# Optimization experiments

Hardware: AMD Instinct MI355X
Metric: run time of the kernel (lower is better)

## Reference

```python
import jax, jax.numpy as jnp
import numpy as np

D_MODEL = 1024
D_HIDDEN = 4096
N_EXPERTS = 8
N_TOKENS = 4096


def setup_inputs() -> dict:
    key = jax.random.key(0)
    ks = jax.random.split(key, 7)
    s = 0.02
    return {
        "x": jax.random.normal(ks[0], (N_TOKENS, D_MODEL), dtype=jnp.float32),
        "gate_w": jax.random.normal(ks[1], (N_EXPERTS, D_MODEL), dtype=jnp.float32) * s,
        "gate_b": jnp.zeros((N_EXPERTS,), dtype=jnp.float32),
        "w1": jax.random.normal(ks[2], (N_EXPERTS, D_MODEL, D_HIDDEN), dtype=jnp.float32) * s,
        "b1": jnp.zeros((N_EXPERTS, D_HIDDEN), dtype=jnp.float32),
        "w2": jax.random.normal(ks[3], (N_EXPERTS, D_HIDDEN, D_MODEL), dtype=jnp.float32) * s,
        "b2": jnp.zeros((N_EXPERTS, D_MODEL), dtype=jnp.float32),
    }


def reference(x, gate_w, gate_b, w1, b1, w2, b2):
    # gate: softmax over expert logits, hard top-1 routing (no prob weighting,
    # matching the torch module which writes the raw expert output back)
    gate_logits = x @ gate_w.T + gate_b                      # [N, E]
    gate_probs = jax.nn.softmax(gate_logits, axis=-1)
    top_expert = jnp.argmax(gate_probs, axis=-1)             # [N] int

    # dense all-expert MLP, then one-hot select (vectorized top-1 MoE)
    h = jax.nn.relu(jnp.einsum('nd,edh->neh', x, w1) + b1[None])  # [N, E, Dh]
    y = jnp.einsum('neh,ehd->ned', h, w2) + b2[None]              # [N, E, D]
    onehot = jax.nn.one_hot(top_expert, N_EXPERTS, dtype=x.dtype)  # [N, E]
    out = jnp.einsum('ned,ne->nd', y, onehot)                      # [N, D]
    return out
```

## Files before the change

kernel.cpp:

```cpp
#include <hip/hip_runtime.h>
#include <hip/hip_bf16.h>

#define NT 4096
#define DM 1024
#define DH 4096
#define NE 8

#define BM 128
#define BN 128
#define BK 32
#define MAXT 40
#define MAXROWS 5120
#define KSPL2 2
#define BKP 40
#define G1B (8 * 4 * MAXT)

typedef short bf16x8 __attribute__((ext_vector_type(8)));
typedef float f32x4 __attribute__((ext_vector_type(4)));
typedef float f4 __attribute__((ext_vector_type(4)));
typedef unsigned short u16x8 __attribute__((ext_vector_type(8)));

#define MI_COUNTS 0
#define MI_POFF   16
#define MI_NTILES 32
#define MI_TILEE  48
#define MI_TILER  112
#define MI_TILES0 176

#define O_BUCKET 1024ull
#define O_XB  (O_BUCKET + (size_t)NE * NT * 4)
#define O_H   (O_XB + (size_t)NT * DM * 2)
#define O_W1T (O_H + (size_t)MAXROWS * DH * 2)
#define O_W2T (O_W1T + (size_t)NE * DM * DH * 2)
#define WS_NEED (O_W2T + (size_t)NE * DH * DM * 2)
#define O_P   O_W1T

static __device__ __forceinline__ unsigned short f2bf(float f) {
  union { __hip_bfloat16 h; unsigned short u; } cv;
  cv.h = __float2bfloat16(f);
  return cv.u;
}

static __device__ __forceinline__ void gload16(const void* g, void* l) {
  __builtin_amdgcn_global_load_lds(
      (const __attribute__((address_space(1))) void*)g,
      (__attribute__((address_space(3))) void*)l, 16, 0, 0);
}

static __device__ __forceinline__ void convert_tile(
    const float* __restrict__ S, __hip_bfloat16* __restrict__ D, int K, int N,
    int k0, int n0, char* smem) {
  auto Ls = reinterpret_cast<__hip_bfloat16(*)[136]>(smem);
  const int tid = threadIdx.x;
  const int c = tid & 15, kq = tid >> 4;
  const float* src = S + (size_t)(k0 + kq * 8) * N + n0 + c * 4;
  f4 v[8];
#pragma unroll
  for (int j = 0; j < 8; ++j) v[j] = *(const f4*)(src + (size_t)j * N);
#pragma unroll
  for (int i = 0; i < 4; ++i) {
    u16x8 w;
#pragma unroll
    for (int j = 0; j < 8; ++j) w[j] = f2bf(v[j][i]);
    *(u16x8*)&Ls[c * 4 + i][kq * 8] = w;
  }
  __syncthreads();
  const int r = tid >> 2, q = tid & 3;
  __hip_bfloat16* drow = D + (size_t)(n0 + r) * K + k0 + q * 32;
#pragma unroll
  for (int u = 0; u < 4; ++u) {
    uint4 w = *(const uint4*)&Ls[r][q * 32 + u * 8];
    *(uint4*)(drow + u * 8) = w;
  }
}

static __device__ __forceinline__ void gate_body(
    const float* __restrict__ x, const float* __restrict__ gw,
    const float* __restrict__ gb, int* __restrict__ counts,
    int* __restrict__ bucket, __hip_bfloat16* __restrict__ xb, int bid) {
  const int tid = threadIdx.x;
  const int wid = tid >> 6;
  const int lane = tid & 63;
  const int t = bid * 4 + wid;

  const f4* xrow = (const f4*)(x + (size_t)t * DM);
  ushort4* xbrow = (ushort4*)(xb + (size_t)t * DM);

  double part[NE];
#pragma unroll
  for (int e = 0; e < NE; ++e) part[e] = 0.0;

#pragma unroll
  for (int q = 0; q < 4; ++q) {
    f4 v = xrow[q * 64 + lane];
    ushort4 s;
    s.x = f2bf(v[0]); s.y = f2bf(v[1]); s.z = f2bf(v[2]); s.w = f2bf(v[3]);
    xbrow[q * 64 + lane] = s;
#pragma unroll
    for (int e = 0; e < NE; ++e) {
      f4 w = ((const f4*)(gw + (size_t)e * DM))[q * 64 + lane];
      part[e] += (double)v[0] * w[0] + (double)v[1] * w[1] +
                 (double)v[2] * w[2] + (double)v[3] * w[3];
    }
  }
#pragma unroll
  for (int off = 32; off; off >>= 1) {
#pragma unroll
    for (int e = 0; e < NE; ++e) part[e] += __shfl_down(part[e], off);
  }
  if (lane == 0) {
    double best = part[0] + (double)gb[0];
    int bi = 0;
#pragma unroll
    for (int e = 1; e < NE; ++e) {
      double le = part[e] + (double)gb[e];
      if (le > best) { best = le; bi = e; }
    }
    int pos = atomicAdd(&counts[bi], 1);
    bucket[bi * NT + pos] = t;
  }
}

__global__ __launch_bounds__(256) void gate_cw1_kernel(
    const float* __restrict__ x, const float* __restrict__ gw,
    const float* __restrict__ gb, int* __restrict__ counts,
    int* __restrict__ bucket, __hip_bfloat16* __restrict__ xb,
    const float* __restrict__ w1, __hip_bfloat16* __restrict__ w1t) {
  __shared__ __align__(16) char smem[17408];
  const int bid = blockIdx.x;
  if (bid < NT / 4) {
    gate_body(x, gw, gb, counts, bucket, xb, bid);
    return;
  }
  const int id = bid - NT / 4;
  const int e = id >> 9, rem = id & 511;
  convert_tile(w1 + (size_t)e * DM * DH, w1t + (size_t)e * DM * DH, DM, DH,
               (rem >> 6) * 128, (rem & 63) * 64, smem);
}

__global__ void prefix_kernel(int* __restrict__ meta, int* __restrict__ bucket) {
  if (threadIdx.x == 0) {
    int r = 0, nt = 0;
    for (int e = 0; e < NE; ++e) {
      meta[MI_POFF + e] = r;
      const int cnt = meta[MI_COUNTS + e];
      const int T = (cnt + BM - 1) / BM;
      for (int j = 0; j < T; ++j) {
        meta[MI_TILEE + nt] = e;
        meta[MI_TILER + nt] = r + j * BM;
        meta[MI_TILES0 + nt] = j * BM;
        ++nt;
      }
      r += T * BM;
    }
    meta[MI_POFF + NE] = r;
    meta[MI_NTILES] = nt;
  }
  __syncthreads();
  for (int e = 0; e < NE; ++e) {
    const int cnt = meta[MI_COUNTS + e];
    if (cnt == 0) continue;
    const int padTo = ((cnt + BM - 1) / BM) * BM;
    const int last = bucket[e * NT + cnt - 1];
    for (int i = cnt + threadIdx.x; i < padTo; i += blockDim.x)
      bucket[e * NT + i] = last;
  }
}

template <int MODE>
static __device__ __forceinline__ void gemm_body(
    char* smem, int b, const __hip_bfloat16* __restrict__ A,
    const __hip_bfloat16* __restrict__ B, const float* __restrict__ biasAll,
    const int* __restrict__ meta, const int* __restrict__ bucket,
    void* __restrict__ Out) {
  auto As = reinterpret_cast<__hip_bfloat16(*)[BM][BK]>(smem);
  auto Bs = reinterpret_cast<__hip_bfloat16(*)[BN][BK]>(smem + 16384);

  const int xcd = b & 7;
  const int idx = b >> 3;
  int tile, ntile, kq;
  if (MODE == 0) {
    const int grp = idx / MAXT;
    tile = idx - grp * MAXT;
    ntile = xcd * 4 + grp;
    kq = 0;
  } else {
    const int grp = idx / MAXT;
    tile = idx - grp * MAXT;
    const int np = xcd * 2 + grp;
    ntile = np >> 1;
    kq = np & 1;
  }
  if (tile >= meta[MI_NTILES]) return;

  const int e = meta[MI_TILEE + tile];
  const int row0 = meta[MI_TILER + tile];
  const int s0 = meta[MI_TILES0 + tile];
  const int n0 = ntile * BN;
  const int Ktot = (MODE == 0) ? DM : DH;
  const int N = (MODE == 0) ? DH : DM;
  const int KTM = (MODE == 0) ? 32 : 64;
  const int kbase = (MODE == 0) ? 0 : kq * (DH / KSPL2);

  const int tid = threadIdx.x;
  const int lane = tid & 63;
  const int wid = tid >> 6;
  const int lr = lane >> 2, lc = lane & 3;

  const __hip_bfloat16 *aP0, *aP1;
  if (MODE == 0) {
    aP0 = A + (size_t)bucket[e * NT + s0 + 32 * wid + lr] * DM + lc * 8;
    aP1 = A + (size_t)bucket[e * NT + s0 + 32 * wid + 16 + lr] * DM + lc * 8;
  } else {
    aP0 = A + (size_t)(row0 + 32 * wid + lr) * DH + kbase + lc * 8;
    aP1 = A + (size_t)(row0 + 32 * wid + 16 + lr) * DH + kbase + lc * 8;
  }
  const __hip_bfloat16* bP0 =
      B + ((size_t)e * N + n0 + 32 * wid + lr) * Ktot + kbase + lc * 8;
  const __hip_bfloat16* bP1 = bP0 + (size_t)16 * Ktot;

  const int wm = (wid >> 1) * 64, wn = (wid & 1) * 64;
  const int fr = lane & 15, ks = lane >> 4;

  f32x4 acc[4][4];
#pragma unroll
  for (int m = 0; m < 4; ++m)
#pragma unroll
    for (int n = 0; n < 4; ++n) acc[m][n] = (f32x4){0.f, 0.f, 0.f, 0.f};

#define STAGE(bf, kt)                                  \
  do {                                                 \
    const size_t ko_ = (size_t)(kt) * BK;              \
    gload16(aP0 + ko_, &As[bf][32 * wid][0]);          \
    gload16(aP1 + ko_, &As[bf][32 * wid + 16][0]);     \
    gload16(bP0 + ko_, &Bs[bf][32 * wid][0]);          \
    gload16(bP1 + ko_, &Bs[bf][32 * wid + 16][0]);     \
  } while (0)

  STAGE(0, 0);
  __syncthreads();

  for (int kt = 0; kt < KTM; ++kt) {
    const int buf = kt & 1;
    if (kt + 1 < KTM) STAGE(buf ^ 1, kt + 1);
    bf16x8 afr[4], bfr[4];
#pragma unroll
    for (int m = 0; m < 4; ++m)
      afr[m] = *(const bf16x8*)&As[buf][wm + m * 16 + fr][ks * 8];
#pragma unroll
    for (int n = 0; n < 4; ++n)
      bfr[n] = *(const bf16x8*)&Bs[buf][wn + n * 16 + fr][ks * 8];
#pragma unroll
    for (int m = 0; m < 4; ++m)
#pragma unroll
      for (int n = 0; n < 4; ++n)
        acc[m][n] = __builtin_amdgcn_mfma_f32_16x16x32_bf16(afr[m], bfr[n],
                                                            acc[m][n], 0, 0, 0);
    __syncthreads();
  }
#undef STAGE

  if (MODE == 0) {
    const float* bias = biasAll + (size_t)e * DH;
    __hip_bfloat16* Hout = (__hip_bfloat16*)Out;
#pragma unroll
    for (int m = 0; m < 4; ++m)
#pragma unroll
      for (int r = 0; r < 4; ++r) {
        const int row = wm + m * 16 + ks * 4 + r;
        __hip_bfloat16* orow = Hout + (size_t)(row0 + row) * DH;
#pragma unroll
        for (int n = 0; n < 4; ++n) {
          const int col = n0 + wn + n * 16 + fr;
          float v = acc[m][n][r] + bias[col];
          orow[col] = __float2bfloat16(v > 0.f ? v : 0.f);
        }
      }
  } else {
    float* Pout = (float*)Out + (size_t)kq * MAXROWS * DM;
#pragma unroll
    for (int m = 0; m < 4; ++m)
#pragma unroll
      for (int r = 0; r < 4; ++r) {
        const int row = wm + m * 16 + ks * 4 + r;
        float* orow = Pout + (size_t)(row0 + row) * DM;
#pragma unroll
        for (int n = 0; n < 4; ++n) {
          const int col = n0 + wn + n * 16 + fr;
          orow[col] = acc[m][n][r];
        }
      }
  }
}

__global__ __launch_bounds__(256, 2) void gemm1_cw2_kernel(
    const __hip_bfloat16* __restrict__ xb, const __hip_bfloat16* __restrict__ w1t,
    const float* __restrict__ b1, const int* __restrict__ meta,
    const int* __restrict__ bucket, __hip_bfloat16* __restrict__ h,
    const float* __restrict__ w2, __hip_bfloat16* __restrict__ w2t) {
  __shared__ __align__(16) char smem[32768];
  const int bid = blockIdx.x;
  if (bid < G1B) {
    gemm_body<0>(smem, bid, xb, w1t, b1, meta, bucket, (void*)h);
    return;
  }
  const int id = bid - G1B;
  const int e = id >> 9, rem = id & 511;
  convert_tile(w2 + (size_t)e * DH * DM, w2t + (size_t)e * DH * DM, DH, DM,
               (rem >> 4) * 128, (rem & 15) * 64, smem);
}

__global__ __launch_bounds__(256, 2) void gemm2_kernel(
    const __hip_bfloat16* __restrict__ h, const __hip_bfloat16* __restrict__ w2t,
    const int* __restrict__ meta, const int* __restrict__ bucket,
    float* __restrict__ P) {
  __shared__ __align__(16) char smem[32768];
  gemm_body<1>(smem, blockIdx.x, h, w2t, nullptr, meta, bucket, (void*)P);
}

__global__ __launch_bounds__(256) void reduce_out_kernel(
    const float* __restrict__ P, const float* __restrict__ b2,
    const int* __restrict__ meta, const int* __restrict__ bucket,
    float* __restrict__ out) {
  const int gs = blockIdx.x;
  if (gs >= meta[MI_POFF + NE]) return;
  int e = 0;
#pragma unroll
  for (int i = 1; i < NE; ++i) e = (gs >= meta[MI_POFF + i]) ? i : e;
  const int i = gs - meta[MI_POFF + e];
  if (i >= meta[MI_COUNTS + e]) return;
  const int tok = bucket[e * NT + i];
  const int c = threadIdx.x * 4;
  float4 v = *(const float4*)(P + (size_t)gs * DM + c);
#pragma unroll
  for (int q = 1; q < KSPL2; ++q) {
    float4 p = *(const float4*)(P + ((size_t)q * MAXROWS + gs) * DM + c);
    v.x += p.x; v.y += p.y; v.z += p.z; v.w += p.w;
  }
  float4 b = *(const float4*)(b2 + (size_t)e * DM + c);
  v.x += b.x; v.y += b.y; v.z += b.z; v.w += b.w;
  *(float4*)(out + (size_t)tok * DM + c) = v;
}

__global__ __launch_bounds__(256) void gate_route_kernel(
    const float* __restrict__ x, const float* __restrict__ gw,
    const float* __restrict__ gb, int* __restrict__ counts,
    int* __restrict__ bucket, __hip_bfloat16* __restrict__ xb) {
  gate_body(x, gw, gb, counts, bucket, xb, blockIdx.x);
}

template <bool RELU_BF16>
__global__ __launch_bounds__(256, 2) void moe_gemm_fallback(
    const __hip_bfloat16* __restrict__ Aall, int lda,
    const float* __restrict__ Ball, int K, int N,
    const float* __restrict__ biasAll, const int* __restrict__ counts,
    const int* __restrict__ bucket, void* __restrict__ Out, int ldo) {
  const int e = blockIdx.z;
  const int cnt = counts[e];
  const int m0 = blockIdx.y * BM;
  if (m0 >= cnt) return;
  const int n0 = blockIdx.x * BN;

  const float* Bp = Ball + (size_t)e * K * N;
  const float* bias = biasAll + (size_t)e * N;
  const int* buck = bucket + e * NT;

  __shared__ __align__(16) __hip_bfloat16 As[2][BM][BKP];
  __shared__ __align__(16) __hip_bfloat16 Bs[2][BN][BKP];

  const int tid = threadIdx.x;
  const int lane = tid & 63;
  const int wid = tid >> 6;
  const int wm = (wid >> 1) * 64;
  const int wn = (wid & 1) * 64;
  const int fr = lane & 15;
  const int ks = lane >> 4;

  const int ar = tid >> 1;
  const int ah = tid & 1;
  const int atok = buck[min(m0 + ar, cnt - 1)];
  const __hip_bfloat16* aptr = Aall + (size_t)atok * lda + ah * 16;

  const int bc = tid & 31;
  const int bk0 = (tid >> 5) * 4;

  f32x4 acc[4][4];
#pragma unroll
  for (int m = 0; m < 4; ++m)
#pragma unroll
    for (int n = 0; n < 4; ++n) acc[m][n] = (f32x4){0.f, 0.f, 0.f, 0.f};

  const int KTf = K / BK;
  uint4 ra0, ra1;
  float rb[4][4];

  {
    const uint4* p = (const uint4*)(aptr);
    ra0 = p[0]; ra1 = p[1];
    const float* bbase = Bp + (size_t)bk0 * N + n0 + bc;
#pragma unroll
    for (int i = 0; i < 4; ++i)
#pragma unroll
      for (int j = 0; j < 4; ++j) rb[i][j] = bbase[(size_t)i * N + 32 * j];
  }
  {
    *(uint4*)&As[0][ar][ah * 16] = ra0;
    *(uint4*)&As[0][ar][ah * 16 + 8] = ra1;
#pragma unroll
    for (int j = 0; j < 4; ++j) {
      ushort4 w;
      w.x = f2bf(rb[0][j]); w.y = f2bf(rb[1][j]);
      w.z = f2bf(rb[2][j]); w.w = f2bf(rb[3][j]);
      *(ushort4*)&Bs[0][bc + 32 * j][bk0] = w;
    }
  }
  __syncthreads();

  for (int kt = 0; kt < KTf; ++kt) {
    const int buf = kt & 1;
    if (kt + 1 < KTf) {
      const uint4* p = (const uint4*)(aptr + (size_t)(kt + 1) * BK);
      ra0 = p[0]; ra1 = p[1];
      const float* bbase = Bp + (size_t)((kt + 1) * BK + bk0) * N + n0 + bc;
#pragma unroll
      for (int i = 0; i < 4; ++i)
#pragma unroll
        for (int j = 0; j < 4; ++j) rb[i][j] = bbase[(size_t)i * N + 32 * j];
    }

    bf16x8 afr[4], bfr[4];
#pragma unroll
    for (int m = 0; m < 4; ++m)
      afr[m] = *(const bf16x8*)&As[buf][wm + m * 16 + fr][ks * 8];
#pragma unroll
    for (int n = 0; n < 4; ++n)
      bfr[n] = *(const bf16x8*)&Bs[buf][wn + n * 16 + fr][ks * 8];
#pragma unroll
    for (int m = 0; m < 4; ++m)
#pragma unroll
      for (int n = 0; n < 4; ++n)
        acc[m][n] = __builtin_amdgcn_mfma_f32_16x16x32_bf16(afr[m], bfr[n],
                                                            acc[m][n], 0, 0, 0);

    __syncthreads();
    if (kt + 1 < KTf) {
      *(uint4*)&As[buf ^ 1][ar][ah * 16] = ra0;
      *(uint4*)&As[buf ^ 1][ar][ah * 16 + 8] = ra1;
#pragma unroll
      for (int j = 0; j < 4; ++j) {
        ushort4 w;
        w.x = f2bf(rb[0][j]); w.y = f2bf(rb[1][j]);
        w.z = f2bf(rb[2][j]); w.w = f2bf(rb[3][j]);
        *(ushort4*)&Bs[buf ^ 1][bc + 32 * j][bk0] = w;
      }
      __syncthreads();
    }
  }

  float* outF = (float*)Out;
  __hip_bfloat16* outB = (__hip_bfloat16*)Out;
#pragma unroll
  for (int m = 0; m < 4; ++m) {
#pragma unroll
    for (int r = 0; r < 4; ++r) {
      const int row = wm + m * 16 + ks * 4 + r;
      const int slot = m0 + row;
      if (slot < cnt) {
        const int tok = buck[slot];
#pragma unroll
        for (int n = 0; n < 4; ++n) {
          const int col = n0 + wn + n * 16 + fr;
          float v = acc[m][n][r] + bias[col];
          if (RELU_BF16) {
            v = v > 0.f ? v : 0.f;
            outB[(size_t)tok * ldo + col] = __float2bfloat16(v);
          } else {
            outF[(size_t)tok * ldo + col] = v;
          }
        }
      }
    }
  }
}

extern "C" void kernel_launch(void* const* d_in, const int* in_sizes, int n_in,
                              void* d_out, int out_size, void* d_ws,
                              size_t ws_size, hipStream_t stream) {
  const float* x = (const float*)d_in[0];
  const float* gw = (const float*)d_in[1];
  const float* gb = (const float*)d_in[2];
  const float* w1 = (const float*)d_in[3];
  const float* b1 = (const float*)d_in[4];
  const float* w2 = (const float*)d_in[5];
  const float* b2 = (const float*)d_in[6];
  (void)in_sizes; (void)n_in; (void)out_size;

  char* ws = (char*)d_ws;
  int* meta = (int*)ws;
  int* counts = meta + MI_COUNTS;
  int* bucket = (int*)(ws + O_BUCKET);
  __hip_bfloat16* xb = (__hip_bfloat16*)(ws + O_XB);
  __hip_bfloat16* h = (__hip_bfloat16*)(ws + O_H);

  hipMemsetAsync(ws, 0, 1024, stream);

  if (ws_size >= WS_NEED) {
    __hip_bfloat16* w1t = (__hip_bfloat16*)(ws + O_W1T);
    __hip_bfloat16* w2t = (__hip_bfloat16*)(ws + O_W2T);
    float* P = (float*)(ws + O_P);

    gate_cw1_kernel<<<NT / 4 + 4096, 256, 0, stream>>>(
        x, gw, gb, counts, bucket, xb, w1, w1t);
    prefix_kernel<<<1, 256, 0, stream>>>(meta, bucket);
    gemm1_cw2_kernel<<<G1B + 4096, 256, 0, stream>>>(
        xb, w1t, b1, meta, bucket, h, w2, w2t);
    gemm2_kernel<<<8 * 2 * MAXT, 256, 0, stream>>>(h, w2t, meta, bucket, P);
    reduce_out_kernel<<<MAXROWS, 256, 0, stream>>>(P, b2, meta, bucket,
                                                   (float*)d_out);
  } else {
    gate_route_kernel<<<NT / 4, 256, 0, stream>>>(x, gw, gb, counts, bucket,
                                                  xb);
    dim3 g1(DH / BN, NT / BM, NE);
    moe_gemm_fallback<true><<<g1, 256, 0, stream>>>(
        xb, DM, w1, DM, DH, b1, counts, bucket, (void*)h, DH);
    dim3 g2(DM / BN, NT / BM, NE);
    moe_gemm_fallback<false><<<g2, 256, 0, stream>>>(
        h, DH, w2, DH, DM, b2, counts, bucket, d_out, DM);
  }
}
```

Baseline: 266.5 us.

## Convert weights in larger 256-K chunks per block and split gate from w1 conversion

The fp32-to-bf16 transpose of w1 and w2 is reworked so each block converts a 128-column strip across 256 K values in four 64-row sub-steps. This cuts the conversion block count from 4096 to 1024 per weight, and each output row write becomes a 64-byte contiguous run per thread pair. Gate routing is moved out of the fused gate+convert kernel into its own launch ahead of a separate cw1 kernel. The aim is fewer blocks, better write coalescing and less per-block overhead, at the cost of one extra kernel launch and reduced parallelism inside the conversion.

```diff
diff --git a/kernel.cpp b/kernel.cpp
--- a/kernel.cpp
+++ b/kernel.cpp
@@ -14,6 +14,7 @@
 #define KSPL2 2
 #define BKP 40
 #define G1B (8 * 4 * MAXT)
+#define KC 256
 
 typedef short bf16x8 __attribute__((ext_vector_type(8)));
 typedef float f32x4 __attribute__((ext_vector_type(4)));
@@ -47,30 +48,33 @@
       (__attribute__((address_space(3))) void*)l, 16, 0, 0);
 }
 
-static __device__ __forceinline__ void convert_tile(
+static __device__ __forceinline__ void convert_v3(
     const float* __restrict__ S, __hip_bfloat16* __restrict__ D, int K, int N,
-    int k0, int n0, char* smem) {
-  auto Ls = reinterpret_cast<__hip_bfloat16(*)[136]>(smem);
+    int kc0, int n0, char* smem) {
   const int tid = threadIdx.x;
-  const int c = tid & 15, kq = tid >> 4;
-  const float* src = S + (size_t)(k0 + kq * 8) * N + n0 + c * 4;
-  f4 v[8];
-#pragma unroll
-  for (int j = 0; j < 8; ++j) v[j] = *(const f4*)(src + (size_t)j * N);
-#pragma unroll
-  for (int i = 0; i < 4; ++i) {
-    u16x8 w;
-#pragma unroll
-    for (int j = 0; j < 8; ++j) w[j] = f2bf(v[j][i]);
-    *(u16x8*)&Ls[c * 4 + i][kq * 8] = w;
-  }
-  __syncthreads();
-  const int r = tid >> 2, q = tid & 3;
-  __hip_bfloat16* drow = D + (size_t)(n0 + r) * K + k0 + q * 32;
-#pragma unroll
-  for (int u = 0; u < 4; ++u) {
-    uint4 w = *(const uint4*)&Ls[r][q * 32 + u * 8];
-    *(uint4*)(drow + u * 8) = w;
+  const int c = tid & 31, kq = tid >> 5;
+  const int r = tid >> 1, q = tid & 1;
+#pragma unroll
+  for (int it = 0; it < KC / 64; ++it) {
+    const int k0 = kc0 + it * 64;
+    const float* src = S + (size_t)(k0 + kq * 8) * N + n0 + c * 4;
+    f4 v[8];
+#pragma unroll
+    for (int j = 0; j < 8; ++j) v[j] = *(const f4*)(src + (size_t)j * N);
+    if (it) __syncthreads();
+#pragma unroll
+    for (int i = 0; i < 4; ++i) {
+      u16x8 w;
+#pragma unroll
+      for (int j = 0; j < 8; ++j) w[j] = f2bf(v[j][i]);
+      *(u16x8*)(smem + (c * 4 + i) * 144 + kq * 16) = w;
+    }
+    __syncthreads();
+    __hip_bfloat16* drow = D + (size_t)(n0 + r) * K + k0 + q * 32;
+#pragma unroll
+    for (int u = 0; u < 4; ++u)
+      *(uint4*)(drow + u * 8) =
+          *(const uint4*)(smem + r * 144 + q * 64 + u * 16);
   }
 }
 
@@ -121,21 +125,23 @@
   }
 }
 
-__global__ __launch_bounds__(256) void gate_cw1_kernel(
+__global__ __launch_bounds__(256) void gate_route_kernel(
     const float* __restrict__ x, const float* __restrict__ gw,
     const float* __restrict__ gb, int* __restrict__ counts,
-    int* __restrict__ bucket, __hip_bfloat16* __restrict__ xb,
+    int* __restrict__ bucket, __hip_bfloat16* __restrict__ xb) {
+  gate_body(x, gw, gb, counts, bucket, xb, blockIdx.x);
+}
+
+__global__ __launch_bounds__(256) void cw1_kernel(
     const float* __restrict__ w1, __hip_bfloat16* __restrict__ w1t) {
-  __shared__ __align__(16) char smem[17408];
-  const int bid = blockIdx.x;
-  if (bid < NT / 4) {
-    gate_body(x, gw, gb, counts, bucket, xb, bid);
-    return;
-  }
-  const int id = bid - NT / 4;
-  const int e = id >> 9, rem = id & 511;
-  convert_tile(w1 + (size_t)e * DM * DH, w1t + (size_t)e * DM * DH, DM, DH,
-               (rem >> 6) * 128, (rem & 63) * 64, smem);
+  __shared__ __align__(16) char smem[18432];
+  const int id = blockIdx.x;
+  const int e = id & 7;
+  const int rem = id >> 3;
+  const int kc = rem & 3;
+  const int nt = rem >> 2;
+  convert_v3(w1 + (size_t)e * DM * DH, w1t + (size_t)e * DM * DH, DM, DH,
+             kc * KC, nt * 128, smem);
 }
 
 __global__ void prefix_kernel(int* __restrict__ meta, int* __restrict__ bucket) {
@@ -305,9 +311,12 @@
     return;
   }
   const int id = bid - G1B;
-  const int e = id >> 9, rem = id & 511;
-  convert_tile(w2 + (size_t)e * DH * DM, w2t + (size_t)e * DH * DM, DH, DM,
-               (rem >> 4) * 128, (rem & 15) * 64, smem);
+  const int e = id & 7;
+  const int rem = id >> 3;
+  const int kc = rem & 15;
+  const int nt = rem >> 4;
+  convert_v3(w2 + (size_t)e * DH * DM, w2t + (size_t)e * DH * DM, DH, DM,
+             kc * KC, nt * 128, smem);
 }
 
 __global__ __launch_bounds__(256, 2) void gemm2_kernel(
@@ -315,7 +324,8 @@
     const int* __restrict__ meta, const int* __restrict__ bucket,
     float* __restrict__ P) {
   __shared__ __align__(16) char smem[32768];
-  gemm_body<1>(smem, blockIdx.x, h, w2t, nullptr, meta, bucket, (void*)P);
+  gemm_body<1>(smem, blockIdx.x, h, w2t, meta ? nullptr : nullptr, meta, bucket,
+               (void*)P);
 }
 
 __global__ __launch_bounds__(256) void reduce_out_kernel(
@@ -340,13 +350,6 @@
   float4 b = *(const float4*)(b2 + (size_t)e * DM + c);
   v.x += b.x; v.y += b.y; v.z += b.z; v.w += b.w;
   *(float4*)(out + (size_t)tok * DM + c) = v;
-}
-
-__global__ __launch_bounds__(256) void gate_route_kernel(
-    const float* __restrict__ x, const float* __restrict__ gw,
-    const float* __restrict__ gb, int* __restrict__ counts,
-    int* __restrict__ bucket, __hip_bfloat16* __restrict__ xb) {
-  gate_body(x, gw, gb, counts, bucket, xb, blockIdx.x);
 }
 
 template <bool RELU_BF16>
@@ -509,10 +512,11 @@
     __hip_bfloat16* w2t = (__hip_bfloat16*)(ws + O_W2T);
     float* P = (float*)(ws + O_P);
 
-    gate_cw1_kernel<<<NT / 4 + 4096, 256, 0, stream>>>(
-        x, gw, gb, counts, bucket, xb, w1, w1t);
+    gate_route_kernel<<<NT / 4, 256, 0, stream>>>(x, gw, gb, counts, bucket,
+                                                  xb);
+    cw1_kernel<<<1024, 256, 0, stream>>>(w1, w1t);
     prefix_kernel<<<1, 256, 0, stream>>>(meta, bucket);
-    gemm1_cw2_kernel<<<G1B + 4096, 256, 0, stream>>>(
+    gemm1_cw2_kernel<<<G1B + 1024, 256, 0, stream>>>(
         xb, w1t, b1, meta, bucket, h, w2, w2t);
     gemm2_kernel<<<8 * 2 * MAXT, 256, 0, stream>>>(h, w2t, meta, bucket, P);
     reduce_out_kernel<<<MAXROWS, 256, 0, stream>>>(P, b2, meta, bucket,
```

Result: slower. 307.7 us (+15.4%).

## Store converted weights in tile-blocked layout for contiguous GEMM B loads

Applied to the files above, without the earlier changes.

The fp32-to-bf16 weight conversion now writes each expert's transposed weights in a blocked layout, with every 128-column by 32-k tile stored as one contiguous 8 KB chunk. GEMM blocks can then fetch their B tile with fully contiguous per-wave loads instead of strided row reads. Conversion blocks are made smaller (64x64 tiles, twice as many blocks) and are interleaved across experts, trading less work and shared memory per block for more launched blocks.

```diff
diff --git a/kernel.cpp b/kernel.cpp
--- a/kernel.cpp
+++ b/kernel.cpp
@@ -18,7 +18,6 @@
 typedef short bf16x8 __attribute__((ext_vector_type(8)));
 typedef float f32x4 __attribute__((ext_vector_type(4)));
 typedef float f4 __attribute__((ext_vector_type(4)));
-typedef unsigned short u16x8 __attribute__((ext_vector_type(8)));
 
 #define MI_COUNTS 0
 #define MI_POFF   16
@@ -47,30 +46,34 @@
       (__attribute__((address_space(3))) void*)l, 16, 0, 0);
 }
 
-static __device__ __forceinline__ void convert_tile(
-    const float* __restrict__ S, __hip_bfloat16* __restrict__ D, int K, int N,
-    int k0, int n0, char* smem) {
-  auto Ls = reinterpret_cast<__hip_bfloat16(*)[136]>(smem);
+static __device__ __forceinline__ void convert_v4(
+    const float* __restrict__ S, __hip_bfloat16* __restrict__ D, int N,
+    int KTcnt, int kglob0, int nglob0, char* smem) {
+  auto Ls = reinterpret_cast<__hip_bfloat16(*)[72]>(smem);
   const int tid = threadIdx.x;
-  const int c = tid & 15, kq = tid >> 4;
-  const float* src = S + (size_t)(k0 + kq * 8) * N + n0 + c * 4;
-  f4 v[8];
-#pragma unroll
-  for (int j = 0; j < 8; ++j) v[j] = *(const f4*)(src + (size_t)j * N);
+  const int c4 = tid & 15, rk = tid >> 4;
+  const float* src = S + (size_t)(kglob0 + rk * 4) * N + nglob0 + c4 * 4;
+  f4 v[4];
+#pragma unroll
+  for (int j = 0; j < 4; ++j) v[j] = *(const f4*)(src + (size_t)j * N);
 #pragma unroll
   for (int i = 0; i < 4; ++i) {
-    u16x8 w;
-#pragma unroll
-    for (int j = 0; j < 8; ++j) w[j] = f2bf(v[j][i]);
-    *(u16x8*)&Ls[c * 4 + i][kq * 8] = w;
+    ushort4 w;
+    w.x = f2bf(v[0][i]); w.y = f2bf(v[1][i]);
+    w.z = f2bf(v[2][i]); w.w = f2bf(v[3][i]);
+    *(ushort4*)&Ls[c4 * 4 + i][rk * 4] = w;
   }
   __syncthreads();
   const int r = tid >> 2, q = tid & 3;
-  __hip_bfloat16* drow = D + (size_t)(n0 + r) * K + k0 + q * 32;
-#pragma unroll
-  for (int u = 0; u < 4; ++u) {
-    uint4 w = *(const uint4*)&Ls[r][q * 32 + u * 8];
-    *(uint4*)(drow + u * 8) = w;
+  const int nt = nglob0 >> 7;
+  const int npr = (nglob0 & 64) + r;
+#pragma unroll
+  for (int u = 0; u < 2; ++u) {
+    const int g = q * 2 + u;
+    const int kt = (kglob0 >> 5) + (g >> 2);
+    uint4 w = *(const uint4*)&Ls[r][g * 8];
+    *(uint4*)(D + ((size_t)nt * KTcnt + kt) * 4096 + npr * 32 + (g & 3) * 8) =
+        w;
   }
 }
 
@@ -126,16 +129,19 @@
     const float* __restrict__ gb, int* __restrict__ counts,
     int* __restrict__ bucket, __hip_bfloat16* __restrict__ xb,
     const float* __restrict__ w1, __hip_bfloat16* __restrict__ w1t) {
-  __shared__ __align__(16) char smem[17408];
+  __shared__ __align__(16) char smem[9216];
   const int bid = blockIdx.x;
   if (bid < NT / 4) {
     gate_body(x, gw, gb, counts, bucket, xb, bid);
     return;
   }
   const int id = bid - NT / 4;
-  const int e = id >> 9, rem = id & 511;
-  convert_tile(w1 + (size_t)e * DM * DH, w1t + (size_t)e * DM * DH, DM, DH,
-               (rem >> 6) * 128, (rem & 63) * 64, smem);
+  const int e = id & 7;
+  const int rem = id >> 3;
+  const int ktg = rem & 15;
+  const int m = rem >> 4;
+  convert_v4(w1 + (size_t)e * DM * DH, w1t + (size_t)e * DM * DH, DH,
+             DM / 32, ktg * 64, m * 64, smem);
 }
 
 __global__ void prefix_kernel(int* __restrict__ meta, int* __restrict__ bucket) {
@@ -197,10 +203,11 @@
   const int row0 = meta[MI_TILER + tile];
   const int s0 = meta[MI_TILES0 + tile];
   const int n0 = ntile * BN;
-  const int Ktot = (MODE == 0) ? DM : DH;
-  const int N = (MODE == 0) ? DH : DM;
   const int KTM = (MODE == 0) ? 32 : 64;
   const int kbase = (MODE == 0) ? 0 : kq * (DH / KSPL2);
+  const int NT1 = (MODE == 0) ? (DH / 128) : (DM / 128);
+  const int KTcnt = (MODE == 0) ? (DM / 32) : (DH / 32);
+  const int ktb = (MODE == 0) ? 0 : kq * 64;
 
   const int tid = threadIdx.x;
   const int lane = tid & 63;
@@ -216,8 +223,9 @@
     aP1 = A + (size_t)(row0 + 32 * wid + 16 + lr) * DH + kbase + lc * 8;
   }
   const __hip_bfloat16* bP0 =
-      B + ((size_t)e * N + n0 + 32 * wid + lr) * Ktot + kbase + lc * 8;
-  const __hip_bfloat16* bP1 = bP0 + (size_t)16 * Ktot;
+      B + (((size_t)e * NT1 + ntile) * KTcnt + ktb) * 4096 + wid * 1024 +
+      lane * 8;
+  const __hip_bfloat16* bP1 = bP0 + 512;
 
   const int wm = (wid >> 1) * 64, wn = (wid & 1) * 64;
   const int fr = lane & 15, ks = lane >> 4;
@@ -228,13 +236,12 @@
 #pragma unroll
     for (int n = 0; n < 4; ++n) acc[m][n] = (f32x4){0.f, 0.f, 0.f, 0.f};
 
-#define STAGE(bf, kt)                                  \
-  do {                                                 \
-    const size_t ko_ = (size_t)(kt) * BK;              \
-    gload16(aP0 + ko_, &As[bf][32 * wid][0]);          \
-    gload16(aP1 + ko_, &As[bf][32 * wid + 16][0]);     \
-    gload16(bP0 + ko_, &Bs[bf][32 * wid][0]);          \
-    gload16(bP1 + ko_, &Bs[bf][32 * wid + 16][0]);     \
+#define STAGE(bf, kt)                                              \
+  do {                                                             \
+    gload16(aP0 + (size_t)(kt) * BK, &As[bf][32 * wid][0]);        \
+    gload16(aP1 + (size_t)(kt) * BK, &As[bf][32 * wid + 16][0]);   \
+    gload16(bP0 + (size_t)(kt) * 4096, &Bs[bf][32 * wid][0]);      \
+    gload16(bP1 + (size_t)(kt) * 4096, &Bs[bf][32 * wid + 16][0]); \
   } while (0)
 
   STAGE(0, 0);
@@ -305,9 +312,12 @@
     return;
   }
   const int id = bid - G1B;
-  const int e = id >> 9, rem = id & 511;
-  convert_tile(w2 + (size_t)e * DH * DM, w2t + (size_t)e * DH * DM, DH, DM,
-               (rem >> 4) * 128, (rem & 15) * 64, smem);
+  const int e = id & 7;
+  const int rem = id >> 3;
+  const int ktg = rem & 63;
+  const int m = rem >> 6;
+  convert_v4(w2 + (size_t)e * DH * DM, w2t + (size_t)e * DH * DM, DM,
+             DH / 32, ktg * 64, m * 64, smem);
 }
 
 __global__ __launch_bounds__(256, 2) void gemm2_kernel(
@@ -509,10 +519,10 @@
     __hip_bfloat16* w2t = (__hip_bfloat16*)(ws + O_W2T);
     float* P = (float*)(ws + O_P);
 
-    gate_cw1_kernel<<<NT / 4 + 4096, 256, 0, stream>>>(
+    gate_cw1_kernel<<<NT / 4 + 8192, 256, 0, stream>>>(
         x, gw, gb, counts, bucket, xb, w1, w1t);
     prefix_kernel<<<1, 256, 0, stream>>>(meta, bucket);
-    gemm1_cw2_kernel<<<G1B + 4096, 256, 0, stream>>>(
+    gemm1_cw2_kernel<<<G1B + 8192, 256, 0, stream>>>(
         xb, w1t, b1, meta, bucket, h, w2, w2t);
     gemm2_kernel<<<8 * 2 * MAXT, 256, 0, stream>>>(h, w2t, meta, bucket, P);
     reduce_out_kernel<<<MAXROWS, 256, 0, stream>>>(P, b2, meta, bucket,
```

Measured after the change: 262.6 us. No clear change (-1.5%).
